# Kernel optimization log

Measured on AMD Instinct MI355X. Metric: run time of the kernel, lower is better.

Reference implementation:

```python
import jax, jax.numpy as jnp
import numpy as np

D_MODEL = 512
SEQ_LEN = 2048
S = 32  # local window size
BATCH = 2


def setup_inputs() -> dict:
    key = jax.random.key(0)
    ks = jax.random.split(key, 12)
    shp = (SEQ_LEN, BATCH, D_MODEL)
    return {
        "query": jax.random.normal(ks[0], shp, jnp.float32),
        "key": jax.random.normal(ks[1], shp, jnp.float32),
        "value": jax.random.normal(ks[2], shp, jnp.float32),
        "Wq": jax.random.normal(ks[3], (D_MODEL, D_MODEL), jnp.float32) * 0.02,
        "bq": jax.random.normal(ks[4], (D_MODEL,), jnp.float32) * 0.01,
        "Wk": jax.random.normal(ks[5], (D_MODEL, D_MODEL), jnp.float32) * 0.02,
        "bk": jax.random.normal(ks[6], (D_MODEL,), jnp.float32) * 0.01,
        "Wv": jax.random.normal(ks[7], (D_MODEL, D_MODEL), jnp.float32) * 0.02,
        "bv": jax.random.normal(ks[8], (D_MODEL,), jnp.float32) * 0.01,
        "pos_bias": jax.random.normal(ks[9], (SEQ_LEN, SEQ_LEN), jnp.float32) * 0.02,
        "Wo": jax.random.normal(ks[10], (D_MODEL, D_MODEL), jnp.float32) * 0.02,
        "bo": jax.random.normal(ks[11], (D_MODEL,), jnp.float32) * 0.01,
    }


def _aft_local(query, key, value, Wq, bq, Wk, bk, Wv, bv, pos_bias, Wo, bo):
    T, B, D = query.shape
    q = query @ Wq.T + bq  # [T,B,D]
    k = key @ Wk.T + bk
    v = value @ Wv.T + bv
    pb = pos_bias[:T, :T]

    # max_logit: elementwise max of per-dim key max and (key + col-max of pos_bias) max,
    # then batch index 0 (faithful to original `[0]` indexing) -> shape [D]
    max_logit = jnp.maximum(k.max(axis=0),
                            (k + pb.max(axis=0)[:, None, None]).max(axis=0))[0]

    # out-of-window running sums: tokens t' <= t - S contribute exp(k) (no pos bias)
    ek = jnp.exp(k - max_logit)                 # [T,B,D]
    cs_num = jnp.cumsum(ek * v, axis=0)
    cs_den = jnp.cumsum(ek, axis=0)
    t_arr = jnp.arange(T)
    prefix_idx = jnp.clip(t_arr - S, 0, T - 1)
    has_prefix = (t_arr >= S)[:, None, None]
    num_out = jnp.where(has_prefix, cs_num[prefix_idx], 0.0)
    den_out = jnp.where(has_prefix, cs_den[prefix_idx], 0.0)

    # in-window part: t' in [max(0, t-S+1), t] with pos_bias[t, t']
    j = jnp.arange(S)
    idx_raw = t_arr[:, None] - S + 1 + j[None, :]   # [T,S]
    valid = (idx_raw >= 0).astype(k.dtype)
    idx = jnp.clip(idx_raw, 0, T - 1)
    k_win = k[idx]                                  # [T,S,B,D]
    v_win = v[idx]                                  # [T,S,B,D]
    pb_win = pb[t_arr[:, None], idx]                # [T,S]
    exp_l = jnp.exp(k_win + pb_win[:, :, None, None] - max_logit) * valid[:, :, None, None]
    num_in = (exp_l * v_win).sum(axis=1)            # [T,B,D]
    den_in = exp_l.sum(axis=1)

    y = jax.nn.sigmoid(q) * (num_out + num_in) / (den_out + den_in)
    return y @ Wo.T + bo


def reference(query, key, value, Wq, bq, Wk, bk, Wv, bv, pos_bias, Wo, bo):
    return _aft_local(query, key, value, Wq, bq, Wk, bk, Wv, bv, pos_bias, Wo, bo)
```

## Files before the change

kernel.cpp:

```cpp
#include <hip/hip_runtime.h>
#include <hip/hip_bf16.h>

#define TT 2048
#define BB 2
#define DD 512
#define BD (BB*DD)
#define SS 32
#define MR (TT*BB)
#define NE (TT*BB*DD)
#define CH 32

typedef __bf16 bf16x8 __attribute__((ext_vector_type(8)));
typedef float f32x4 __attribute__((ext_vector_type(4)));
typedef float f32x2 __attribute__((ext_vector_type(2)));

__device__ __forceinline__ void async_copy16(void* lds, const void* gptr) {
    __builtin_amdgcn_global_load_lds(
        (const __attribute__((address_space(1))) void*)gptr,
        (__attribute__((address_space(3))) void*)lds,
        16, 0, 0);
}

#define MFMA16(a,b,c) __builtin_amdgcn_mfma_f32_16x16x32_bf16((a),(b),(c),0,0,0)

__global__ __launch_bounds__(256) void cast_all(
    const float* __restrict__ s0, const float* __restrict__ s1, const float* __restrict__ s2,
    const float* __restrict__ w0, const float* __restrict__ w1,
    const float* __restrict__ w2, const float* __restrict__ w3,
    __hip_bfloat16* __restrict__ d0, __hip_bfloat16* __restrict__ d1, __hip_bfloat16* __restrict__ d2,
    __hip_bfloat16* __restrict__ e0, __hip_bfloat16* __restrict__ e1,
    __hip_bfloat16* __restrict__ e2, __hip_bfloat16* __restrict__ e3)
{
    int b = blockIdx.x;
    const float* s;
    __hip_bfloat16* d;
    size_t i;
    if (b < 6144) {
        int which = b >> 11;
        s = which == 0 ? s0 : (which == 1 ? s1 : s2);
        d = which == 0 ? d0 : (which == 1 ? d1 : d2);
        i = ((size_t)(b & 2047) * 256 + threadIdx.x) * 4;
    } else {
        int b2 = b - 6144;
        int which = b2 >> 8;
        s = which == 0 ? w0 : (which == 1 ? w1 : (which == 2 ? w2 : w3));
        d = which == 0 ? e0 : (which == 1 ? e1 : (which == 2 ? e2 : e3));
        i = ((size_t)(b2 & 255) * 256 + threadIdx.x) * 4;
    }
    float4 f = *(const float4*)(s + i);
    union { __hip_bfloat16 h[4]; ushort4 u; } cv;
    cv.h[0] = __float2bfloat16(f.x); cv.h[1] = __float2bfloat16(f.y);
    cv.h[2] = __float2bfloat16(f.z); cv.h[3] = __float2bfloat16(f.w);
    *(ushort4*)((unsigned short*)d + i) = cv.u;
}

__global__ __launch_bounds__(256) void gemm_qkv(
    const __hip_bfloat16* __restrict__ qb, const __hip_bfloat16* __restrict__ kb,
    const __hip_bfloat16* __restrict__ vb,
    const __hip_bfloat16* __restrict__ Wqb, const __hip_bfloat16* __restrict__ Wkb,
    const __hip_bfloat16* __restrict__ Wvb,
    const float* __restrict__ bq, const float* __restrict__ bk,
    const float* __restrict__ bv,
    float* __restrict__ qout, float* __restrict__ ekn,
    float* __restrict__ part)
{
    __shared__ char smem[49152];
    const int tid = threadIdx.x;
    const int lane = tid & 63;
    const int wv = tid >> 6;
    const int wave_m = wv >> 1, wave_n = wv & 1;
    const int m0 = blockIdx.y * 64, n0 = blockIdx.x * 64;
    const int kq = lane >> 4, rr = lane & 15;

    if (blockIdx.z == 0) {
        f32x4 acc[2][2] = {};
        const __hip_bfloat16* Arow = qb + (size_t)(m0 + lane) * DD + wv * 8;
        const __hip_bfloat16* Wrow = Wqb + (size_t)(n0 + lane) * DD + wv * 8;
        async_copy16(smem + 0*8192 +        wv*1024, Arow + 0);
        async_copy16(smem + 0*8192 + 4096 + wv*1024, Wrow + 0);
        async_copy16(smem + 1*8192 +        wv*1024, Arow + 32);
        async_copy16(smem + 1*8192 + 4096 + wv*1024, Wrow + 32);
        asm volatile("s_waitcnt vmcnt(2)" ::: "memory");
        __builtin_amdgcn_s_barrier();
        #pragma unroll
        for (int it = 0; it < 16; ++it) {
            if (it + 2 < 16) {
                char* nb = smem + ((it + 2) % 3) * 8192;
                async_copy16(nb +        wv*1024, Arow + (it+2)*32);
                async_copy16(nb + 4096 + wv*1024, Wrow + (it+2)*32);
            }
            const char* cb = smem + (it % 3) * 8192;
            bf16x8 a0 = *(const bf16x8*)(cb + kq*1024 + (wave_m*32 +  0 + rr)*16);
            bf16x8 a1 = *(const bf16x8*)(cb + kq*1024 + (wave_m*32 + 16 + rr)*16);
            bf16x8 w0 = *(const bf16x8*)(cb + 4096 + kq*1024 + (wave_n*32 +  0 + rr)*16);
            bf16x8 w1 = *(const bf16x8*)(cb + 4096 + kq*1024 + (wave_n*32 + 16 + rr)*16);
            acc[0][0] = MFMA16(a0, w0, acc[0][0]);
            acc[0][1] = MFMA16(a0, w1, acc[0][1]);
            acc[1][0] = MFMA16(a1, w0, acc[1][0]);
            acc[1][1] = MFMA16(a1, w1, acc[1][1]);
            if (it < 15) {
                if (it < 14) asm volatile("s_waitcnt vmcnt(2) lgkmcnt(0)" ::: "memory");
                else         asm volatile("s_waitcnt vmcnt(0) lgkmcnt(0)" ::: "memory");
                __builtin_amdgcn_s_barrier();
            }
        }
        #pragma unroll
        for (int ms = 0; ms < 2; ++ms)
            #pragma unroll
            for (int ns = 0; ns < 2; ++ns) {
                int n = n0 + wave_n*32 + ns*16 + rr;
                float bn = bq[n];
                #pragma unroll
                for (int r = 0; r < 4; ++r) {
                    int m = m0 + wave_m*32 + ms*16 + kq*4 + r;
                    qout[(size_t)m * DD + n] = acc[ms][ns][r] + bn;
                }
            }
    } else {
        f32x4 acck[2][2] = {}, accv[2][2] = {};
        const __hip_bfloat16* AKrow = kb + (size_t)(m0 + lane) * DD + wv * 8;
        const __hip_bfloat16* WKrow = Wkb + (size_t)(n0 + lane) * DD + wv * 8;
        const __hip_bfloat16* AVrow = vb + (size_t)(m0 + lane) * DD + wv * 8;
        const __hip_bfloat16* WVrow = Wvb + (size_t)(n0 + lane) * DD + wv * 8;
        #pragma unroll
        for (int pt = 0; pt < 2; ++pt) {
            char* nb = smem + pt * 16384;
            async_copy16(nb +         wv*1024, AKrow + pt*32);
            async_copy16(nb +  4096 + wv*1024, WKrow + pt*32);
            async_copy16(nb +  8192 + wv*1024, AVrow + pt*32);
            async_copy16(nb + 12288 + wv*1024, WVrow + pt*32);
        }
        asm volatile("s_waitcnt vmcnt(4)" ::: "memory");
        __builtin_amdgcn_s_barrier();
        #pragma unroll
        for (int it = 0; it < 16; ++it) {
            if (it + 2 < 16) {
                char* nb = smem + ((it + 2) % 3) * 16384;
                async_copy16(nb +         wv*1024, AKrow + (it+2)*32);
                async_copy16(nb +  4096 + wv*1024, WKrow + (it+2)*32);
                async_copy16(nb +  8192 + wv*1024, AVrow + (it+2)*32);
                async_copy16(nb + 12288 + wv*1024, WVrow + (it+2)*32);
            }
            const char* cb = smem + (it % 3) * 16384;
            bf16x8 ak0 = *(const bf16x8*)(cb +         kq*1024 + (wave_m*32 +  0 + rr)*16);
            bf16x8 ak1 = *(const bf16x8*)(cb +         kq*1024 + (wave_m*32 + 16 + rr)*16);
            bf16x8 bk0 = *(const bf16x8*)(cb +  4096 + kq*1024 + (wave_n*32 +  0 + rr)*16);
            bf16x8 bk1 = *(const bf16x8*)(cb +  4096 + kq*1024 + (wave_n*32 + 16 + rr)*16);
            bf16x8 av0 = *(const bf16x8*)(cb +  8192 + kq*1024 + (wave_m*32 +  0 + rr)*16);
            bf16x8 av1 = *(const bf16x8*)(cb +  8192 + kq*1024 + (wave_m*32 + 16 + rr)*16);
            bf16x8 bv0 = *(const bf16x8*)(cb + 12288 + kq*1024 + (wave_n*32 +  0 + rr)*16);
            bf16x8 bv1 = *(const bf16x8*)(cb + 12288 + kq*1024 + (wave_n*32 + 16 + rr)*16);
            acck[0][0] = MFMA16(ak0, bk0, acck[0][0]);
            acck[0][1] = MFMA16(ak0, bk1, acck[0][1]);
            acck[1][0] = MFMA16(ak1, bk0, acck[1][0]);
            acck[1][1] = MFMA16(ak1, bk1, acck[1][1]);
            accv[0][0] = MFMA16(av0, bv0, accv[0][0]);
            accv[0][1] = MFMA16(av0, bv1, accv[0][1]);
            accv[1][0] = MFMA16(av1, bv0, accv[1][0]);
            accv[1][1] = MFMA16(av1, bv1, accv[1][1]);
            if (it < 15) {
                if (it < 14) asm volatile("s_waitcnt vmcnt(4) lgkmcnt(0)" ::: "memory");
                else         asm volatile("s_waitcnt vmcnt(0) lgkmcnt(0)" ::: "memory");
                __builtin_amdgcn_s_barrier();
            }
        }
        float sd[2][2] = {{0.f,0.f},{0.f,0.f}};
        float sn[2][2] = {{0.f,0.f},{0.f,0.f}};
        #pragma unroll
        for (int ms = 0; ms < 2; ++ms)
            #pragma unroll
            for (int ns = 0; ns < 2; ++ns) {
                int n = n0 + wave_n*32 + ns*16 + rr;
                float bkn = bk[n], bvn = bv[n];
                #pragma unroll
                for (int r = 0; r < 4; ++r) {
                    int m = m0 + wave_m*32 + ms*16 + kq*4 + r;
                    float e  = expf(acck[ms][ns][r] + bkn);
                    float nv = e * (accv[ms][ns][r] + bvn);
                    float2 st; st.x = e; st.y = nv;
                    *(float2*)&ekn[((size_t)m * DD + n) * 2] = st;
                    sd[ns][r & 1] += e;
                    sn[ns][r & 1] += nv;
                }
            }
        #pragma unroll
        for (int ns = 0; ns < 2; ++ns)
            #pragma unroll
            for (int par = 0; par < 2; ++par) {
                sd[ns][par] += __shfl_xor(sd[ns][par], 16, 64);
                sd[ns][par] += __shfl_xor(sd[ns][par], 32, 64);
                sn[ns][par] += __shfl_xor(sn[ns][par], 16, 64);
                sn[ns][par] += __shfl_xor(sn[ns][par], 32, 64);
            }
        __syncthreads();
        float* red = (float*)smem;
        if (lane < 16) {
            #pragma unroll
            for (int ns = 0; ns < 2; ++ns) {
                int c = wave_n*32 + ns*16 + rr;
                red[(0*2 + wave_m)*64 + c] = sd[ns][0];
                red[(1*2 + wave_m)*64 + c] = sd[ns][1];
                red[(2*2 + wave_m)*64 + c] = sn[ns][0];
                red[(3*2 + wave_m)*64 + c] = sn[ns][1];
            }
        }
        __syncthreads();
        {
            int which = tid >> 6;
            int c = tid & 63;
            float s = red[(which*2 + 0)*64 + c] + red[(which*2 + 1)*64 + c];
            int b = which & 1;
            int sel = which >> 1;
            part[((size_t)blockIdx.y * BD + b*512 + n0 + c) * 2 + sel] = s;
        }
    }
}

__global__ __launch_bounds__(256, 1) void scan_part(
    const float* __restrict__ part, float* __restrict__ pref)
{
    const int col = blockIdx.x * 256 + threadIdx.x;
    f32x2 run = {0.f, 0.f};
    #pragma unroll
    for (int p0 = 0; p0 < 64; p0 += 8) {
        f32x2 v[8];
        #pragma unroll
        for (int u = 0; u < 8; ++u)
            v[u] = *(const f32x2*)&part[((size_t)(p0 + u) * BD + col) * 2];
        #pragma unroll
        for (int u = 0; u < 8; ++u) {
            *(f32x2*)&pref[((size_t)(p0 + u) * BD + col) * 2] = run;
            run += v[u];
        }
    }
}

__global__ __launch_bounds__(256, 1) void fused_window(
    const float* __restrict__ q, const float* __restrict__ ekn,
    const float* __restrict__ pref, const float* __restrict__ pb,
    __hip_bfloat16* __restrict__ yb)
{
    __shared__ float wl[CH][SS];
    const int tid = threadIdx.x;
    const int col = blockIdx.x * 256 + tid;
    const int chunk = blockIdx.y;
    const int t0 = chunk * CH;

    f32x2 E[64];
    if (chunk > 0) {
        #pragma unroll
        for (int i = 0; i < 64; ++i)
            E[i] = *(const f32x2*)&ekn[((size_t)(t0 - 32 + i) * BD + col) * 2];
    } else {
        #pragma unroll
        for (int i = 0; i < 32; ++i) E[i] = (f32x2){0.f, 0.f};
        #pragma unroll
        for (int i = 32; i < 64; ++i)
            E[i] = *(const f32x2*)&ekn[((size_t)(t0 - 32 + i) * BD + col) * 2];
    }
    f32x2 P = *(const f32x2*)&pref[((size_t)chunk * BD + col) * 2];
    float qv[CH];
    #pragma unroll
    for (int s = 0; s < CH; ++s)
        qv[s] = q[(size_t)(t0 + s) * BD + col];

    #pragma unroll
    for (int i = 0; i < (CH * SS) / 256; ++i) {
        int idx = tid + i * 256;
        int tl = idx >> 5, j = idx & 31;
        int t = t0 + tl;
        int u = t - (SS - 1) + j;
        float w = 0.f;
        if (u >= 0) w = expf(pb[(size_t)t * TT + u]);
        wl[tl][j] = w;
    }
    __syncthreads();

    f32x2 cs = P;
    #pragma unroll
    for (int i = 0; i < 32; ++i) cs -= E[i];

    #pragma unroll
    for (int s = 0; s < CH; ++s) {
        cs += E[s];
        f32x2 acc = cs;
        #pragma unroll
        for (int j4 = 0; j4 < 8; ++j4) {
            float4 w4 = *(const float4*)&wl[s][j4 * 4];
            acc += w4.x * E[s + 1 + j4*4 + 0];
            acc += w4.y * E[s + 1 + j4*4 + 1];
            acc += w4.z * E[s + 1 + j4*4 + 2];
            acc += w4.w * E[s + 1 + j4*4 + 3];
        }
        float sig = 1.f / (1.f + expf(-qv[s]));
        yb[(size_t)(t0 + s) * BD + col] = __float2bfloat16(sig * acc.y / acc.x);
    }
}

__global__ __launch_bounds__(256) void gemm_out(
    const __hip_bfloat16* __restrict__ yb, const __hip_bfloat16* __restrict__ Wob,
    const float* __restrict__ bo, float* __restrict__ out)
{
    __shared__ char smem[24576];
    const int tid = threadIdx.x;
    const int lane = tid & 63;
    const int wv = tid >> 6;
    const int wave_m = wv >> 1, wave_n = wv & 1;
    const int m0 = blockIdx.y * 64, n0 = blockIdx.x * 64;
    const int kq = lane >> 4, rr = lane & 15;

    f32x4 acc[2][2] = {};
    const __hip_bfloat16* Arow = yb + (size_t)(m0 + lane) * DD + wv * 8;
    const __hip_bfloat16* Wrow = Wob + (size_t)(n0 + lane) * DD + wv * 8;

    async_copy16(smem + 0*8192 +        wv*1024, Arow + 0);
    async_copy16(smem + 0*8192 + 4096 + wv*1024, Wrow + 0);
    async_copy16(smem + 1*8192 +        wv*1024, Arow + 32);
    async_copy16(smem + 1*8192 + 4096 + wv*1024, Wrow + 32);
    asm volatile("s_waitcnt vmcnt(2)" ::: "memory");
    __builtin_amdgcn_s_barrier();
    #pragma unroll
    for (int it = 0; it < 16; ++it) {
        if (it + 2 < 16) {
            char* nb = smem + ((it + 2) % 3) * 8192;
            async_copy16(nb +        wv*1024, Arow + (it+2)*32);
            async_copy16(nb + 4096 + wv*1024, Wrow + (it+2)*32);
        }
        const char* cb = smem + (it % 3) * 8192;
        bf16x8 a0 = *(const bf16x8*)(cb + kq*1024 + (wave_m*32 +  0 + rr)*16);
        bf16x8 a1 = *(const bf16x8*)(cb + kq*1024 + (wave_m*32 + 16 + rr)*16);
        bf16x8 w0 = *(const bf16x8*)(cb + 4096 + kq*1024 + (wave_n*32 +  0 + rr)*16);
        bf16x8 w1 = *(const bf16x8*)(cb + 4096 + kq*1024 + (wave_n*32 + 16 + rr)*16);
        acc[0][0] = MFMA16(a0, w0, acc[0][0]);
        acc[0][1] = MFMA16(a0, w1, acc[0][1]);
        acc[1][0] = MFMA16(a1, w0, acc[1][0]);
        acc[1][1] = MFMA16(a1, w1, acc[1][1]);
        if (it < 15) {
            if (it < 14) asm volatile("s_waitcnt vmcnt(2) lgkmcnt(0)" ::: "memory");
            else         asm volatile("s_waitcnt vmcnt(0) lgkmcnt(0)" ::: "memory");
            __builtin_amdgcn_s_barrier();
        }
    }
    #pragma unroll
    for (int ms = 0; ms < 2; ++ms)
        #pragma unroll
        for (int ns = 0; ns < 2; ++ns) {
            int n = n0 + wave_n*32 + ns*16 + rr;
            float bn = bo[n];
            #pragma unroll
            for (int r = 0; r < 4; ++r) {
                int m = m0 + wave_m*32 + ms*16 + kq*4 + r;
                out[(size_t)m * DD + n] = acc[ms][ns][r] + bn;
            }
        }
}

extern "C" void kernel_launch(void* const* d_in, const int* in_sizes, int n_in,
                              void* d_out, int out_size, void* d_ws, size_t ws_size,
                              hipStream_t stream) {
    const float* query = (const float*)d_in[0];
    const float* key   = (const float*)d_in[1];
    const float* value = (const float*)d_in[2];
    const float* Wq    = (const float*)d_in[3];
    const float* bq    = (const float*)d_in[4];
    const float* Wk    = (const float*)d_in[5];
    const float* bk    = (const float*)d_in[6];
    const float* Wv    = (const float*)d_in[7];
    const float* bv    = (const float*)d_in[8];
    const float* pb    = (const float*)d_in[9];
    const float* Wo    = (const float*)d_in[10];
    const float* bo    = (const float*)d_in[11];
    float* out = (float*)d_out;

    float* ws = (float*)d_ws;
    float* q    = ws;
    float* ekn  = ws + (size_t)NE;
    float* part = ws + (size_t)3 * NE;
    float* pref = part + 131072;
    __hip_bfloat16* bfb = (__hip_bfloat16*)(pref + 131072);
    __hip_bfloat16* qb  = bfb;
    __hip_bfloat16* kb  = bfb + (size_t)NE;
    __hip_bfloat16* vb  = bfb + (size_t)2 * NE;
    __hip_bfloat16* yb  = bfb + (size_t)3 * NE;
    __hip_bfloat16* Wqb = bfb + (size_t)4 * NE;
    __hip_bfloat16* Wkb = Wqb + 262144;
    __hip_bfloat16* Wvb = Wkb + 262144;
    __hip_bfloat16* Wob = Wvb + 262144;

    cast_all<<<7168, 256, 0, stream>>>(query, key, value, Wq, Wk, Wv, Wo,
                                       qb, kb, vb, Wqb, Wkb, Wvb, Wob);

    gemm_qkv<<<dim3(DD / 64, MR / 64, 2), 256, 0, stream>>>(
        qb, kb, vb, Wqb, Wkb, Wvb, bq, bk, bv,
        q, ekn, part);

    scan_part<<<4, 256, 0, stream>>>(part, pref);

    fused_window<<<dim3(BD / 256, TT / CH), 256, 0, stream>>>(
        q, ekn, pref, pb, yb);

    gemm_out<<<dim3(DD / 64, MR / 64), 256, 0, stream>>>(yb, Wob, bo, out);
}
```

Baseline: 172.3 us.

## Restructure window kernel: stage exp(k) tile in LDS and split time rows across waves

The window kernel used to have each thread hold 64 timesteps of exp(k)/exp(k)*v in registers for a single column, with 4 blocks per chunk in x. Now each block covers 64 columns. The 64x64 tile of pairs is loaded into LDS with async global-to-LDS copies, and each of the 4 waves handles 8 timesteps using a 39-entry register ring. The goal is to cut register pressure so occupancy can rise (launch bounds 3), and to launch four times as many blocks. The cost is more LDS traffic and some redundant recomputation of the prefix correction per wave.

```diff
diff --git a/kernel.cpp b/kernel.cpp
--- a/kernel.cpp
+++ b/kernel.cpp
@@ -197,21 +197,21 @@
         if (lane < 16) {
             #pragma unroll
             for (int ns = 0; ns < 2; ++ns) {
-                int c = wave_n*32 + ns*16 + rr;
-                red[(0*2 + wave_m)*64 + c] = sd[ns][0];
-                red[(1*2 + wave_m)*64 + c] = sd[ns][1];
-                red[(2*2 + wave_m)*64 + c] = sn[ns][0];
-                red[(3*2 + wave_m)*64 + c] = sn[ns][1];
+                int c2 = wave_n*32 + ns*16 + rr;
+                red[(0*2 + wave_m)*64 + c2] = sd[ns][0];
+                red[(1*2 + wave_m)*64 + c2] = sd[ns][1];
+                red[(2*2 + wave_m)*64 + c2] = sn[ns][0];
+                red[(3*2 + wave_m)*64 + c2] = sn[ns][1];
             }
         }
         __syncthreads();
         {
             int which = tid >> 6;
-            int c = tid & 63;
-            float s = red[(which*2 + 0)*64 + c] + red[(which*2 + 1)*64 + c];
+            int c2 = tid & 63;
+            float s = red[(which*2 + 0)*64 + c2] + red[(which*2 + 1)*64 + c2];
             int b = which & 1;
             int sel = which >> 1;
-            part[((size_t)blockIdx.y * BD + b*512 + n0 + c) * 2 + sel] = s;
+            part[((size_t)blockIdx.y * BD + b*512 + n0 + c2) * 2 + sel] = s;
         }
     }
 }
@@ -235,65 +235,85 @@
     }
 }
 
-__global__ __launch_bounds__(256, 1) void fused_window(
+__global__ __launch_bounds__(256, 3) void fused_window(
     const float* __restrict__ q, const float* __restrict__ ekn,
     const float* __restrict__ pref, const float* __restrict__ pb,
     __hip_bfloat16* __restrict__ yb)
 {
+    __shared__ float Et[64 * 64 * 2];
     __shared__ float wl[CH][SS];
     const int tid = threadIdx.x;
-    const int col = blockIdx.x * 256 + tid;
     const int chunk = blockIdx.y;
     const int t0 = chunk * CH;
-
-    f32x2 E[64];
-    if (chunk > 0) {
-        #pragma unroll
-        for (int i = 0; i < 64; ++i)
-            E[i] = *(const f32x2*)&ekn[((size_t)(t0 - 32 + i) * BD + col) * 2];
-    } else {
-        #pragma unroll
-        for (int i = 0; i < 32; ++i) E[i] = (f32x2){0.f, 0.f};
-        #pragma unroll
-        for (int i = 32; i < 64; ++i)
-            E[i] = *(const f32x2*)&ekn[((size_t)(t0 - 32 + i) * BD + col) * 2];
-    }
-    f32x2 P = *(const f32x2*)&pref[((size_t)chunk * BD + col) * 2];
-    float qv[CH];
-    #pragma unroll
-    for (int s = 0; s < CH; ++s)
-        qv[s] = q[(size_t)(t0 + s) * BD + col];
+    const int col0 = blockIdx.x * 64;
+    const int c = tid & 63;
+    const int sg = tid >> 6;
+    const int s0 = sg * 8;
+
+    {
+        const int ub = tid >> 5;
+        const int cp = tid & 31;
+        #pragma unroll
+        for (int j = 0; j < 8; ++j) {
+            int u = ub + j * 8;
+            int t = t0 - 32 + u;
+            if (t >= 0) {
+                const void* g = (const void*)(ekn + ((size_t)t * BD + col0 + cp * 2) * 2);
+                async_copy16((char*)Et + (tid >> 6) * 1024 + j * 4096, g);
+            }
+        }
+        if (chunk == 0) {
+            f32x4 z = {0.f, 0.f, 0.f, 0.f};
+            #pragma unroll
+            for (int j = 0; j < 4; ++j)
+                *(f32x4*)((char*)Et + tid * 16 + j * 4096) = z;
+        }
+    }
 
     #pragma unroll
     for (int i = 0; i < (CH * SS) / 256; ++i) {
         int idx = tid + i * 256;
-        int tl = idx >> 5, j = idx & 31;
+        int tl = idx >> 5, jj = idx & 31;
         int t = t0 + tl;
-        int u = t - (SS - 1) + j;
+        int u2 = t - (SS - 1) + jj;
         float w = 0.f;
-        if (u >= 0) w = expf(pb[(size_t)t * TT + u]);
-        wl[tl][j] = w;
-    }
+        if (u2 >= 0) w = expf(pb[(size_t)t * TT + u2]);
+        wl[tl][jj] = w;
+    }
+
+    float qv[8];
+    #pragma unroll
+    for (int k = 0; k < 8; ++k)
+        qv[k] = q[(size_t)(t0 + s0 + k) * BD + col0 + c];
+    f32x2 P = *(const f32x2*)&pref[((size_t)chunk * BD + col0 + c) * 2];
+
     __syncthreads();
 
+    f32x2 ring[39];
+    #pragma unroll
+    for (int i = 0; i < 39; ++i)
+        ring[i] = *(const f32x2*)&Et[((s0 + 1 + i) * 64 + c) * 2];
+
     f32x2 cs = P;
     #pragma unroll
-    for (int i = 0; i < 32; ++i) cs -= E[i];
-
-    #pragma unroll
-    for (int s = 0; s < CH; ++s) {
-        cs += E[s];
+    for (int u = 0; u < 31; ++u)
+        if (u >= s0) cs -= ring[u - s0];
+
+    #pragma unroll
+    for (int k = 0; k < 8; ++k) {
+        int s = s0 + k;
+        if (k > 0) cs += ring[k - 1];
         f32x2 acc = cs;
         #pragma unroll
         for (int j4 = 0; j4 < 8; ++j4) {
             float4 w4 = *(const float4*)&wl[s][j4 * 4];
-            acc += w4.x * E[s + 1 + j4*4 + 0];
-            acc += w4.y * E[s + 1 + j4*4 + 1];
-            acc += w4.z * E[s + 1 + j4*4 + 2];
-            acc += w4.w * E[s + 1 + j4*4 + 3];
-        }
-        float sig = 1.f / (1.f + expf(-qv[s]));
-        yb[(size_t)(t0 + s) * BD + col] = __float2bfloat16(sig * acc.y / acc.x);
+            acc += w4.x * ring[k + j4*4 + 0];
+            acc += w4.y * ring[k + j4*4 + 1];
+            acc += w4.z * ring[k + j4*4 + 2];
+            acc += w4.w * ring[k + j4*4 + 3];
+        }
+        float sig = 1.f / (1.f + expf(-qv[k]));
+        yb[(size_t)(t0 + s) * BD + col0 + c] = __float2bfloat16(sig * acc.y / acc.x);
     }
 }
 
@@ -396,7 +416,7 @@
 
     scan_part<<<4, 256, 0, stream>>>(part, pref);
 
-    fused_window<<<dim3(BD / 256, TT / CH), 256, 0, stream>>>(
+    fused_window<<<dim3(BD / 64, TT / CH), 256, 0, stream>>>(
         q, ekn, pref, pb, yb);
 
     gemm_out<<<dim3(DD / 64, MR / 64), 256, 0, stream>>>(yb, Wob, bo, out);
```

Result: slower. 190.3 us (+10.5%).
